# Performance work log

Measured on AMD Instinct MI355X. Metric: run time of the kernel, lower is better.

Reference implementation:

```python
import jax, jax.numpy as jnp
import numpy as np

LAMBDA_INIT = 0.8


def setup_inputs() -> dict:
    key = jax.random.key(0)
    ks = jax.random.split(key, 12)
    B, T, E = 2, 2048, 1024
    H = 8            # num_heads // 2 diff-heads
    HS = 64          # head_size
    DO = 128         # 2 * head_output_dimension (per-head output dim)
    q = jax.random.normal(ks[0], (B, T, E), jnp.float32)
    k = jax.random.normal(ks[1], (B, T, E), jnp.float32)
    v = jax.random.normal(ks[2], (B, T, E), jnp.float32)
    s = E ** -0.5  # linear-layer style init scale
    Wq = jax.random.normal(ks[3], (H, E, 2 * HS), jnp.float32) * s
    Wk = jax.random.normal(ks[4], (H, E, 2 * HS), jnp.float32) * s
    Wv = jax.random.normal(ks[5], (H, E, DO), jnp.float32) * s
    # lambda reparam vectors (scaled 0.1 to keep exp(dot) numerically tame)
    lq1 = jax.random.normal(ks[6], (H, HS), jnp.float32) * 0.1
    lk1 = jax.random.normal(ks[7], (H, HS), jnp.float32) * 0.1
    lq2 = jax.random.normal(ks[8], (H, HS), jnp.float32) * 0.1
    lk2 = jax.random.normal(ks[9], (H, HS), jnp.float32) * 0.1
    Wp = jax.random.normal(ks[10], (H * DO, E), jnp.float32) * (H * DO) ** -0.5
    bp = jnp.zeros((E,), jnp.float32)
    # buffer: tril(ones, diagonal=1); positions where it is 0 get -inf
    mask = jnp.tril(jnp.ones((T, T), jnp.bool_), 1)
    return {"q": q, "k": k, "v": v, "Wq": Wq, "Wk": Wk, "Wv": Wv,
            "lq1": lq1, "lk1": lk1, "lq2": lq2, "lk2": lk2,
            "Wp": Wp, "bp": bp, "mask": mask}


def reference(q, k, v, Wq, Wk, Wv, lq1, lk1, lq2, lk2, Wp, bp, mask):
    B, T, E = q.shape
    H = Wq.shape[0]
    HS = Wq.shape[-1] // 2
    scale = HS ** -0.5
    Q = jnp.einsum('bte,hed->bhtd', q, Wq)   # [B,H,T,2HS]
    K = jnp.einsum('bte,hed->bhtd', k, Wk)
    V = jnp.einsum('bte,hed->bhtd', v, Wv)   # [B,H,T,DO]
    Q1, Q2 = jnp.split(Q, 2, axis=-1)
    K1, K2 = jnp.split(K, 2, axis=-1)
    neg_inf = jnp.float32(-jnp.inf)
    s1 = jnp.einsum('bhtd,bhsd->bhts', Q1, K1) * scale
    s2 = jnp.einsum('bhtd,bhsd->bhts', Q2, K2) * scale
    s1 = jnp.where(mask[:T, :T], s1, neg_inf)
    s2 = jnp.where(mask[:T, :T], s2, neg_inf)
    a1 = jax.nn.softmax(s1, axis=-1)
    a2 = jax.nn.softmax(s2, axis=-1)
    lbd = (jnp.exp(jnp.sum(lq1 * lk1, -1)) - jnp.exp(jnp.sum(lq2 * lk2, -1))
           + LAMBDA_INIT)                     # [H]
    attn = a1 - lbd[None, :, None, None] * a2
    ctx = jnp.einsum('bhts,bhsd->bhtd', attn, V) * (1.0 - LAMBDA_INIT)
    out = ctx.transpose(0, 2, 1, 3).reshape(B, T, -1)  # concat heads
    return out @ Wp + bp
```

## Files before the change

kernel.cpp:

```cpp
#include <hip/hip_runtime.h>
#include <hip/hip_bf16.h>


constexpr int Tn = 2048;
constexpr int En = 1024;
constexpr int Hn = 8;
constexpr float LAMBDA_INIT = 0.8f;
constexpr float QSCALE = 0.18033688011112042f;

typedef __attribute__((ext_vector_type(8))) short short8;
typedef __attribute__((ext_vector_type(4))) short s16x4;
typedef __attribute__((ext_vector_type(4))) float f32x4;

__device__ __forceinline__ short f2bf(float x) {
  union { __hip_bfloat16 h; short s; } u;
  u.h = __float2bfloat16(x);
  return u.s;
}
__device__ __forceinline__ void gload16(const short* g, short* l) {
  __builtin_amdgcn_global_load_lds(
      (const __attribute__((address_space(1))) void*)g,
      (__attribute__((address_space(3))) void*)l, 16, 0, 0);
}

__global__ __launch_bounds__(256)
void qkv_mfma(const float* __restrict__ q, const float* __restrict__ k,
              const float* __restrict__ v,
              const float* __restrict__ Wq, const float* __restrict__ Wk,
              const float* __restrict__ Wv,
              short* __restrict__ Qo, short* __restrict__ Ko,
              short* __restrict__ Vto) {
  __shared__ short As[2][128 * 32];
  __shared__ short Bs[2][128 * 32];
  const int which = blockIdx.z;
  const float* X = (which == 0) ? q : (which == 1) ? k : v;
  const float* W = (which == 0) ? Wq : (which == 1) ? Wk : Wv;
  const int head = blockIdx.y;
  const int m0 = blockIdx.x * 128;
  const float* Wh = W + (size_t)head * En * 128;
  const float oscale = (which == 0) ? QSCALE : 1.0f;

  const int tid = threadIdx.x;
  const int lane = tid & 63;
  const int w = tid >> 6, wr = w >> 1, wc = w & 1;
  const int fr = lane & 15, fk = (lane >> 4) * 8;
  const int arow = tid >> 1, ah = (tid & 1) * 16;
  const int bn = tid & 127, bkg = (tid >> 7) * 16;

  float4 xa[4];
  float xb[16];

  auto gload = [&](int k0) {
#pragma unroll
    for (int qq = 0; qq < 4; ++qq)
      xa[qq] = *(const float4*)&X[(size_t)(m0 + arow) * En + k0 + ah + qq * 4];
#pragma unroll
    for (int j = 0; j < 16; ++j)
      xb[j] = Wh[(size_t)(k0 + bkg + j) * 128 + bn];
  };
  auto cvtwrite = [&](int buf) {
    short8 pa0, pa1;
#pragma unroll
    for (int e = 0; e < 4; ++e) {
      pa0[e]     = f2bf(((const float*)&xa[0])[e]);
      pa0[e + 4] = f2bf(((const float*)&xa[1])[e]);
      pa1[e]     = f2bf(((const float*)&xa[2])[e]);
      pa1[e + 4] = f2bf(((const float*)&xa[3])[e]);
    }
    *(short8*)&As[buf][arow * 32 + ah] = pa0;
    *(short8*)&As[buf][arow * 32 + ah + 8] = pa1;
    short8 pb0, pb1;
#pragma unroll
    for (int e = 0; e < 8; ++e) {
      pb0[e] = f2bf(xb[e]);
      pb1[e] = f2bf(xb[e + 8]);
    }
    *(short8*)&Bs[buf][bn * 32 + bkg] = pb0;
    *(short8*)&Bs[buf][bn * 32 + bkg + 8] = pb1;
  };

  f32x4 acc[4][4] = {};
  gload(0);
  cvtwrite(0);
  gload(32);
  __syncthreads();

  for (int k0 = 0; k0 < En; k0 += 32) {
    const int cur = (k0 >> 5) & 1;
    if (k0 + 32 < En) {
      cvtwrite(cur ^ 1);
      if (k0 + 64 < En) gload(k0 + 64);
    }
    short8 a[4], b[4];
#pragma unroll
    for (int i = 0; i < 4; ++i)
      a[i] = *(const short8*)&As[cur][(wr * 64 + i * 16 + fr) * 32 + fk];
#pragma unroll
    for (int j = 0; j < 4; ++j)
      b[j] = *(const short8*)&Bs[cur][(wc * 64 + j * 16 + fr) * 32 + fk];
#pragma unroll
    for (int i = 0; i < 4; ++i)
#pragma unroll
      for (int j = 0; j < 4; ++j)
        acc[i][j] = __builtin_amdgcn_mfma_f32_16x16x32_bf16(a[i], b[j],
                                                            acc[i][j], 0, 0, 0);
    __syncthreads();
  }

  const int crow = (lane >> 4) * 4, ccol = lane & 15;
  if (which == 2) {
#pragma unroll
    for (int i = 0; i < 4; ++i) {
      const int m = m0 + wr * 64 + i * 16 + crow;
      const int bb = m >> 11, t = m & (Tn - 1);
#pragma unroll
      for (int j = 0; j < 4; ++j) {
        const int d = wc * 64 + j * 16 + ccol;
        s16x4 pk;
#pragma unroll
        for (int p = 0; p < 4; ++p) pk[p] = f2bf(acc[i][j][p]);
        *(s16x4*)&Vto[((size_t)(bb * Hn + head) * 128 + d) * Tn + t] = pk;
      }
    }
  } else {
    short* Out = (which == 0) ? Qo : Ko;
#pragma unroll
    for (int i = 0; i < 4; ++i) {
      const int m = m0 + wr * 64 + i * 16 + crow;
      const int bb = m >> 11, t = m & (Tn - 1);
      short* dst = Out + ((size_t)(bb * Hn + head) * Tn + t) * 128;
#pragma unroll
      for (int j = 0; j < 4; ++j) {
        const int d = wc * 64 + j * 16 + ccol;
#pragma unroll
        for (int p = 0; p < 4; ++p)
          dst[(size_t)p * 128 + d] = f2bf(acc[i][j][p] * oscale);
      }
    }
  }
}

__global__ __launch_bounds__(256)
void proj_mfma(const short* __restrict__ Xb, const float* __restrict__ W,
               const float* __restrict__ bias, float* __restrict__ Out) {
  __shared__ short As[2][64 * 32];
  __shared__ short Bs[2][128 * 32];
  const int m0 = blockIdx.x * 64;
  const int n0 = blockIdx.y * 128;

  const int tid = threadIdx.x;
  const int lane = tid & 63;
  const int w = tid >> 6, wr = w >> 1, wc = w & 1;
  const int fr = lane & 15, fk = (lane >> 4) * 8;
  const int arow = tid >> 2, ah = (tid & 3) * 8;
  const int bn = tid & 127, bkg = (tid >> 7) * 16;

  short8 xa8;
  float xb[16];

  auto gload = [&](int k0) {
    xa8 = *(const short8*)&Xb[(size_t)(m0 + arow) * En + k0 + ah];
#pragma unroll
    for (int j = 0; j < 16; ++j)
      xb[j] = W[(size_t)(k0 + bkg + j) * En + n0 + bn];
  };
  auto cvtwrite = [&](int buf) {
    *(short8*)&As[buf][arow * 32 + ah] = xa8;
    short8 pb0, pb1;
#pragma unroll
    for (int e = 0; e < 8; ++e) {
      pb0[e] = f2bf(xb[e]);
      pb1[e] = f2bf(xb[e + 8]);
    }
    *(short8*)&Bs[buf][bn * 32 + bkg] = pb0;
    *(short8*)&Bs[buf][bn * 32 + bkg + 8] = pb1;
  };

  f32x4 acc[2][4] = {};
  gload(0);
  cvtwrite(0);
  gload(32);
  __syncthreads();

  for (int k0 = 0; k0 < En; k0 += 32) {
    const int cur = (k0 >> 5) & 1;
    if (k0 + 32 < En) {
      cvtwrite(cur ^ 1);
      if (k0 + 64 < En) gload(k0 + 64);
    }
    short8 a[2], b[4];
#pragma unroll
    for (int i = 0; i < 2; ++i)
      a[i] = *(const short8*)&As[cur][(wr * 32 + i * 16 + fr) * 32 + fk];
#pragma unroll
    for (int j = 0; j < 4; ++j)
      b[j] = *(const short8*)&Bs[cur][(wc * 64 + j * 16 + fr) * 32 + fk];
#pragma unroll
    for (int i = 0; i < 2; ++i)
#pragma unroll
      for (int j = 0; j < 4; ++j)
        acc[i][j] = __builtin_amdgcn_mfma_f32_16x16x32_bf16(a[i], b[j],
                                                            acc[i][j], 0, 0, 0);
    __syncthreads();
  }

  const int crow = (lane >> 4) * 4, ccol = lane & 15;
#pragma unroll
  for (int i = 0; i < 2; ++i) {
    const int m = m0 + wr * 32 + i * 16 + crow;
#pragma unroll
    for (int j = 0; j < 4; ++j) {
      const int n = n0 + wc * 64 + j * 16 + ccol;
      const float bv = bias[n];
#pragma unroll
      for (int p = 0; p < 4; ++p)
        Out[(size_t)(m + p) * En + n] = acc[i][j][p] + bv;
    }
  }
}

__global__ __launch_bounds__(256, 4)
void diff_attn7(const short* __restrict__ Qg, const short* __restrict__ Kg,
                const short* __restrict__ Vtg,
                const float* __restrict__ lq1, const float* __restrict__ lk1,
                const float* __restrict__ lq2, const float* __restrict__ lk2,
                short* __restrict__ ctxb) {
  __shared__ __align__(16) short pool[18688];

  const int lin = blockIdx.x;
  const int h = lin & 7;
  const int idx = lin >> 3;
  const int b = idx >> 5;
  const int x = idx & 31;
  const int tid = threadIdx.x;
  const int lane = tid & 63;
  const int w = tid >> 6;
  const int st = w >> 1, wh = w & 1;
  const int fr = lane & 15, hi = lane >> 4;
  const int swz = fr & 7;
  const int swv = (fr ^ (fr >> 2)) & 3;
  const size_t basebh = (size_t)(b * Hn + h) * Tn * 128;

  float lbd;
  {
    float a1 = lq1[h * 64 + lane] * lk1[h * 64 + lane];
    float a2 = lq2[h * 64 + lane] * lk2[h * 64 + lane];
#pragma unroll
    for (int off = 1; off <= 32; off <<= 1) {
      a1 += __shfl_xor(a1, off);
      a2 += __shfl_xor(a2, off);
    }
    lbd = __expf(a1) - __expf(a2) + LAMBDA_INIT;
  }

  int ksrc[2], vsrc[2], dsto[2];
#pragma unroll
  for (int j = 0; j < 2; ++j) {
    const int ob = j * 4096 + tid * 16;
    { const int s = ob >> 8, cp = (ob >> 4) & 15, c = cp ^ (s & 7);
      ksrc[j] = s * 128 + c * 8; }
    { const int d = ob >> 6, cp = (ob >> 4) & 3,
          c = cp ^ ((d ^ (d >> 2)) & 3);
      vsrc[j] = d * Tn + c * 8; }
    dsto[j] = (j * 4096 + w * 1024) >> 1;
  }
  const short* kgb = Kg + basebh;
  const short* vgb = Vtg + basebh;

#define STAGE(BUF, S0)                                                   \
  {                                                                      \
    const short* kb_ = kgb + (size_t)(S0) * 128;                         \
    const short* vb_ = vgb + (S0);                                       \
    _Pragma("unroll") for (int j = 0; j < 2; ++j) {                      \
      gload16(kb_ + ksrc[j], pool + (BUF) * 4096 + dsto[j]);             \
      gload16(vb_ + vsrc[j], pool + 8192 + (BUF) * 4096 + dsto[j]);      \
    }                                                                    \
  }

  short8 ones;
#pragma unroll
  for (int e = 0; e < 8; ++e) ones[e] = (short)0x3F80;
  short* Plw = pool + 16384 + w * 576;

  auto phase = [&](int qi) {
    const int q0 = qi * 32;
    const int NT = min(Tn / 32, qi + 2);
    const int tmin = q0 + wh * 16;
    const int tbase = tmin + hi * 4;

    short8 qf[2];
    {
      const short* qp = Qg + basebh + (size_t)(tmin + fr) * 128 + st * 64;
      qf[0] = *(const short8*)(qp + hi * 8);
      qf[1] = *(const short8*)(qp + 32 + hi * 8);
    }
    f32x4 o[8] = {};
    f32x4 ol = {};

    STAGE(0, 0);
    int cur = 0;
    for (int t = 0; t < NT; ++t) {
      const int s0 = t * 32;
      if (t + 1 < NT) {
        STAGE(cur ^ 1, s0 + 32);
        __builtin_amdgcn_sched_barrier(0);
        asm volatile("s_waitcnt vmcnt(4)" ::: "memory");
        __builtin_amdgcn_sched_barrier(0);
      } else {
        __builtin_amdgcn_sched_barrier(0);
        asm volatile("s_waitcnt vmcnt(0)" ::: "memory");
        __builtin_amdgcn_sched_barrier(0);
      }
      __builtin_amdgcn_s_barrier();

      if (s0 <= tmin + 16) {
        const short* Kb = pool + cur * 4096;
        const short* Vb = pool + 8192 + cur * 4096;
        const bool interior = (tmin - s0) >= 30;

        f32x4 s4[2] = {};
        __builtin_amdgcn_s_setprio(1);
#pragma unroll
        for (int sb = 0; sb < 2; ++sb) {
          const int rb = (sb * 16 + fr) * 128;
#pragma unroll
          for (int kp = 0; kp < 2; ++kp) {
            const short8 kb = *(const short8*)
                &Kb[rb + ((st * 8 + ((kp * 4 + hi) ^ swz)) << 3)];
            s4[sb] = __builtin_amdgcn_mfma_f32_16x16x32_bf16(qf[kp], kb,
                                                             s4[sb], 0, 0, 0);
          }
        }
        __builtin_amdgcn_s_setprio(0);
        if (!interior) {
#pragma unroll
          for (int sb = 0; sb < 2; ++sb) {
            const int sg = s0 + sb * 16 + fr;
#pragma unroll
            for (int p = 0; p < 4; ++p)
              if (sg > tbase + p + 1) s4[sb][p] = -1e30f;
          }
        }

#pragma unroll
        for (int sb = 0; sb < 2; ++sb)
#pragma unroll
          for (int p = 0; p < 4; ++p)
            Plw[(hi * 4 + p) * 36 + sb * 16 + fr] =
                f2bf(exp2f(s4[sb][p] - 12.0f));

        const short8 pf = *(const short8*)&Plw[fr * 36 + hi * 8];
        __builtin_amdgcn_s_setprio(1);
        ol = __builtin_amdgcn_mfma_f32_16x16x32_bf16(ones, pf, ol, 0, 0, 0);
#pragma unroll
        for (int dblk = 0; dblk < 8; ++dblk) {
          const short8 va = *(const short8*)
              &Vb[(dblk * 16 + fr) * 32 + ((hi ^ swv) << 3)];
          o[dblk] = __builtin_amdgcn_mfma_f32_16x16x32_bf16(va, pf, o[dblk],
                                                            0, 0, 0);
        }
        __builtin_amdgcn_s_setprio(0);
      }

      __builtin_amdgcn_s_barrier();
      cur ^= 1;
    }

    const float lr = ol[0];
    float* O2L = (float*)pool;
    if (st == 1) {
      const float c2 = (1.0f - LAMBDA_INIT) * lbd / lr;
#pragma unroll
      for (int dblk = 0; dblk < 8; ++dblk)
#pragma unroll
        for (int e = 0; e < 4; ++e)
          O2L[wh * 2176 + (dblk * 16 + hi * 4 + e) * 17 + fr] =
              c2 * o[dblk][e];
    }
    __syncthreads();
    if (st == 0) {
      const float c1 = (1.0f - LAMBDA_INIT) / lr;
      const int t = tmin + fr;
      short* dst = ctxb + ((size_t)b * Tn + t) * En + h * 128;
#pragma unroll
      for (int dblk = 0; dblk < 8; ++dblk) {
        s16x4 pk;
#pragma unroll
        for (int e = 0; e < 4; ++e)
          pk[e] = f2bf(c1 * o[dblk][e] -
                       O2L[wh * 2176 + (dblk * 16 + hi * 4 + e) * 17 + fr]);
        *(s16x4*)&dst[dblk * 16 + hi * 4] = pk;
      }
    }
    __syncthreads();
  };

  phase(63 - x);
  phase(x);
#undef STAGE
}

extern "C" void kernel_launch(void* const* d_in, const int* in_sizes, int n_in,
                              void* d_out, int out_size, void* d_ws, size_t ws_size,
                              hipStream_t stream) {
  const float* q   = (const float*)d_in[0];
  const float* k   = (const float*)d_in[1];
  const float* v   = (const float*)d_in[2];
  const float* Wq  = (const float*)d_in[3];
  const float* Wk  = (const float*)d_in[4];
  const float* Wv  = (const float*)d_in[5];
  const float* lq1 = (const float*)d_in[6];
  const float* lk1 = (const float*)d_in[7];
  const float* lq2 = (const float*)d_in[8];
  const float* lk2 = (const float*)d_in[9];
  const float* Wp  = (const float*)d_in[10];
  const float* bp  = (const float*)d_in[11];

  short* ws = (short*)d_ws;
  const size_t SZ = (size_t)2 * Hn * Tn * 128;
  short* Qb   = ws;
  short* Kb   = ws + SZ;
  short* Vtb  = ws + 2 * SZ;
  short* ctxb = ws + 3 * SZ;

  qkv_mfma<<<dim3(32, 8, 3), dim3(256), 0, stream>>>(q, k, v, Wq, Wk, Wv,
                                                     Qb, Kb, Vtb);
  diff_attn7<<<dim3(512), dim3(256), 0, stream>>>(Qb, Kb, Vtb,
                                                  lq1, lk1, lq2, lk2, ctxb);
  proj_mfma<<<dim3(64, 8), dim3(256), 0, stream>>>(ctxb, Wp, bp,
                                                   (float*)d_out);
}
```

Baseline: 161.3 us.

## Pre-convert inputs and weights to bf16, use direct global-to-LDS loads in GEMMs

Adds two prepass kernels: one converts q/k/v activations to bf16, and one transposes and converts all weight matrices to bf16 in K-contiguous layout. The QKV and projection GEMMs then stream tiles straight into LDS with global_load_lds, using explicit vmcnt waits and raw barriers, instead of loading fp32 into registers, converting and writing to LDS. This removes the uncoalesced strided weight loads and per-tile conversion work from the GEMM inner loops. In exchange it adds two extra launches and extra global traffic for the bf16 copies, and the weight conversion is redone on every call.

```diff
diff --git a/kernel.cpp b/kernel.cpp
--- a/kernel.cpp
+++ b/kernel.cpp
@@ -7,6 +7,8 @@
 constexpr int Hn = 8;
 constexpr float LAMBDA_INIT = 0.8f;
 constexpr float QSCALE = 0.18033688011112042f;
+constexpr size_t SZb = (size_t)2 * Tn * En;
+constexpr size_t WSZ = (size_t)En * En;
 
 typedef __attribute__((ext_vector_type(8))) short short8;
 typedef __attribute__((ext_vector_type(4))) short s16x4;
@@ -24,88 +26,132 @@
 }
 
 __global__ __launch_bounds__(256)
-void qkv_mfma(const float* __restrict__ q, const float* __restrict__ k,
-              const float* __restrict__ v,
-              const float* __restrict__ Wq, const float* __restrict__ Wk,
-              const float* __restrict__ Wv,
-              short* __restrict__ Qo, short* __restrict__ Ko,
-              short* __restrict__ Vto) {
-  __shared__ short As[2][128 * 32];
-  __shared__ short Bs[2][128 * 32];
+void cvt3(const float* __restrict__ q, const float* __restrict__ k,
+          const float* __restrict__ v, short* __restrict__ ws) {
+  const float* src = (blockIdx.y == 0) ? q : (blockIdx.y == 1) ? k : v;
+  short* dst = ws + (size_t)blockIdx.y * SZb;
+  const size_t i = ((size_t)blockIdx.x * 256 + threadIdx.x) * 8;
+  float4 a = *(const float4*)&src[i];
+  float4 b = *(const float4*)&src[i + 4];
+  short8 o;
+  o[0] = f2bf(a.x); o[1] = f2bf(a.y); o[2] = f2bf(a.z); o[3] = f2bf(a.w);
+  o[4] = f2bf(b.x); o[5] = f2bf(b.y); o[6] = f2bf(b.z); o[7] = f2bf(b.w);
+  *(short8*)&dst[i] = o;
+}
+
+__global__ __launch_bounds__(256)
+void twt(const float* __restrict__ Wq, const float* __restrict__ Wk,
+         const float* __restrict__ Wv, const float* __restrict__ Wp,
+         short* __restrict__ WT) {
+  __shared__ float tl[64][65];
+  const int id = blockIdx.x;
+  const int tid = threadIdx.x;
+  const float* src;
+  short* dst;
+  int r0, c0, C;
+  if (id < 768) {
+    const int wi = id >> 8;
+    const float* W = (wi == 0) ? Wq : (wi == 1) ? Wk : Wv;
+    const int rem = id & 255;
+    const int h = rem >> 5;
+    const int tile = rem & 31;
+    r0 = (tile >> 1) * 64;
+    c0 = (tile & 1) * 64;
+    C = 128;
+    src = W + (size_t)h * En * 128;
+    dst = WT + (size_t)wi * WSZ + (size_t)h * 128 * En;
+  } else {
+    const int idx = id - 768;
+    r0 = (idx >> 4) * 64;
+    c0 = (idx & 15) * 64;
+    C = En;
+    src = Wp;
+    dst = WT + 3 * WSZ;
+  }
+  const int r = tid >> 2, cc = (tid & 3) * 16;
+#pragma unroll
+  for (int j = 0; j < 4; ++j) {
+    const float4 x = *(const float4*)&src[(size_t)(r0 + r) * C + c0 + cc + j * 4];
+    tl[r][cc + j * 4 + 0] = x.x;
+    tl[r][cc + j * 4 + 1] = x.y;
+    tl[r][cc + j * 4 + 2] = x.z;
+    tl[r][cc + j * 4 + 3] = x.w;
+  }
+  __syncthreads();
+  const int c = tid >> 2, rc = (tid & 3) * 16;
+  short8 o0, o1;
+#pragma unroll
+  for (int e = 0; e < 8; ++e) {
+    o0[e] = f2bf(tl[rc + e][c]);
+    o1[e] = f2bf(tl[rc + 8 + e][c]);
+  }
+  *(short8*)&dst[(size_t)(c0 + c) * En + r0 + rc] = o0;
+  *(short8*)&dst[(size_t)(c0 + c) * En + r0 + rc + 8] = o1;
+}
+
+__global__ __launch_bounds__(256)
+void qkv_mfma2(const short* __restrict__ Xq, const short* __restrict__ Xk,
+               const short* __restrict__ Xv, const short* __restrict__ WT,
+               short* __restrict__ Qo, short* __restrict__ Ko,
+               short* __restrict__ Vto) {
+  __shared__ __align__(16) short As[2][4096];
+  __shared__ __align__(16) short Bs2[2][4096];
   const int which = blockIdx.z;
-  const float* X = (which == 0) ? q : (which == 1) ? k : v;
-  const float* W = (which == 0) ? Wq : (which == 1) ? Wk : Wv;
+  const short* X = (which == 0) ? Xq : (which == 1) ? Xk : Xv;
   const int head = blockIdx.y;
   const int m0 = blockIdx.x * 128;
-  const float* Wh = W + (size_t)head * En * 128;
+  const short* Bt = WT + (size_t)which * WSZ + (size_t)head * 128 * En;
   const float oscale = (which == 0) ? QSCALE : 1.0f;
 
   const int tid = threadIdx.x;
   const int lane = tid & 63;
   const int w = tid >> 6, wr = w >> 1, wc = w & 1;
   const int fr = lane & 15, fk = (lane >> 4) * 8;
-  const int arow = tid >> 1, ah = (tid & 1) * 16;
-  const int bn = tid & 127, bkg = (tid >> 7) * 16;
-
-  float4 xa[4];
-  float xb[16];
-
-  auto gload = [&](int k0) {
-#pragma unroll
-    for (int qq = 0; qq < 4; ++qq)
-      xa[qq] = *(const float4*)&X[(size_t)(m0 + arow) * En + k0 + ah + qq * 4];
-#pragma unroll
-    for (int j = 0; j < 16; ++j)
-      xb[j] = Wh[(size_t)(k0 + bkg + j) * 128 + bn];
-  };
-  auto cvtwrite = [&](int buf) {
-    short8 pa0, pa1;
-#pragma unroll
-    for (int e = 0; e < 4; ++e) {
-      pa0[e]     = f2bf(((const float*)&xa[0])[e]);
-      pa0[e + 4] = f2bf(((const float*)&xa[1])[e]);
-      pa1[e]     = f2bf(((const float*)&xa[2])[e]);
-      pa1[e + 4] = f2bf(((const float*)&xa[3])[e]);
-    }
-    *(short8*)&As[buf][arow * 32 + ah] = pa0;
-    *(short8*)&As[buf][arow * 32 + ah + 8] = pa1;
-    short8 pb0, pb1;
-#pragma unroll
-    for (int e = 0; e < 8; ++e) {
-      pb0[e] = f2bf(xb[e]);
-      pb1[e] = f2bf(xb[e + 8]);
-    }
-    *(short8*)&Bs[buf][bn * 32 + bkg] = pb0;
-    *(short8*)&Bs[buf][bn * 32 + bkg + 8] = pb1;
-  };
+  const int srow = tid >> 2, sch = (tid & 3) * 8;
+  const int wdst = w * 512;
+
+#define QSTAGE(BUF, K0)                                                  \
+  {                                                                      \
+    _Pragma("unroll") for (int j = 0; j < 2; ++j) {                      \
+      gload16(&X[(size_t)(m0 + j * 64 + srow) * En + (K0) + sch],        \
+              &As[BUF][j * 2048 + wdst]);                                \
+      gload16(&Bt[(size_t)(j * 64 + srow) * En + (K0) + sch],            \
+              &Bs2[BUF][j * 2048 + wdst]);                               \
+    }                                                                    \
+  }
 
   f32x4 acc[4][4] = {};
-  gload(0);
-  cvtwrite(0);
-  gload(32);
-  __syncthreads();
-
+  QSTAGE(0, 0);
   for (int k0 = 0; k0 < En; k0 += 32) {
     const int cur = (k0 >> 5) & 1;
     if (k0 + 32 < En) {
-      cvtwrite(cur ^ 1);
-      if (k0 + 64 < En) gload(k0 + 64);
-    }
+      QSTAGE(cur ^ 1, k0 + 32);
+      __builtin_amdgcn_sched_barrier(0);
+      asm volatile("s_waitcnt vmcnt(4)" ::: "memory");
+      __builtin_amdgcn_sched_barrier(0);
+    } else {
+      __builtin_amdgcn_sched_barrier(0);
+      asm volatile("s_waitcnt vmcnt(0)" ::: "memory");
+      __builtin_amdgcn_sched_barrier(0);
+    }
+    __builtin_amdgcn_s_barrier();
+
     short8 a[4], b[4];
 #pragma unroll
     for (int i = 0; i < 4; ++i)
       a[i] = *(const short8*)&As[cur][(wr * 64 + i * 16 + fr) * 32 + fk];
 #pragma unroll
     for (int j = 0; j < 4; ++j)
-      b[j] = *(const short8*)&Bs[cur][(wc * 64 + j * 16 + fr) * 32 + fk];
+      b[j] = *(const short8*)&Bs2[cur][(wc * 64 + j * 16 + fr) * 32 + fk];
 #pragma unroll
     for (int i = 0; i < 4; ++i)
 #pragma unroll
       for (int j = 0; j < 4; ++j)
         acc[i][j] = __builtin_amdgcn_mfma_f32_16x16x32_bf16(a[i], b[j],
                                                             acc[i][j], 0, 0, 0);
-    __syncthreads();
-  }
+    __builtin_amdgcn_s_barrier();
+  }
+#undef QSTAGE
 
   const int crow = (lane >> 4) * 4, ccol = lane & 15;
   if (which == 2) {
@@ -141,10 +187,10 @@
 }
 
 __global__ __launch_bounds__(256)
-void proj_mfma(const short* __restrict__ Xb, const float* __restrict__ W,
-               const float* __restrict__ bias, float* __restrict__ Out) {
-  __shared__ short As[2][64 * 32];
-  __shared__ short Bs[2][128 * 32];
+void proj_mfma2(const short* __restrict__ Xb, const short* __restrict__ WpT,
+                const float* __restrict__ bias, float* __restrict__ Out) {
+  __shared__ __align__(16) short As[2][2048];
+  __shared__ __align__(16) short Bs2[2][4096];
   const int m0 = blockIdx.x * 64;
   const int n0 = blockIdx.y * 128;
 
@@ -152,57 +198,50 @@
   const int lane = tid & 63;
   const int w = tid >> 6, wr = w >> 1, wc = w & 1;
   const int fr = lane & 15, fk = (lane >> 4) * 8;
-  const int arow = tid >> 2, ah = (tid & 3) * 8;
-  const int bn = tid & 127, bkg = (tid >> 7) * 16;
-
-  short8 xa8;
-  float xb[16];
-
-  auto gload = [&](int k0) {
-    xa8 = *(const short8*)&Xb[(size_t)(m0 + arow) * En + k0 + ah];
-#pragma unroll
-    for (int j = 0; j < 16; ++j)
-      xb[j] = W[(size_t)(k0 + bkg + j) * En + n0 + bn];
-  };
-  auto cvtwrite = [&](int buf) {
-    *(short8*)&As[buf][arow * 32 + ah] = xa8;
-    short8 pb0, pb1;
-#pragma unroll
-    for (int e = 0; e < 8; ++e) {
-      pb0[e] = f2bf(xb[e]);
-      pb1[e] = f2bf(xb[e + 8]);
-    }
-    *(short8*)&Bs[buf][bn * 32 + bkg] = pb0;
-    *(short8*)&Bs[buf][bn * 32 + bkg + 8] = pb1;
-  };
+  const int srow = tid >> 2, sch = (tid & 3) * 8;
+  const int wdst = w * 512;
+
+#define PSTAGE(BUF, K0)                                                  \
+  {                                                                      \
+    gload16(&Xb[(size_t)(m0 + srow) * En + (K0) + sch],                  \
+            &As[BUF][wdst]);                                             \
+    _Pragma("unroll") for (int j = 0; j < 2; ++j)                        \
+      gload16(&WpT[(size_t)(n0 + j * 64 + srow) * En + (K0) + sch],      \
+              &Bs2[BUF][j * 2048 + wdst]);                               \
+  }
 
   f32x4 acc[2][4] = {};
-  gload(0);
-  cvtwrite(0);
-  gload(32);
-  __syncthreads();
-
+  PSTAGE(0, 0);
   for (int k0 = 0; k0 < En; k0 += 32) {
     const int cur = (k0 >> 5) & 1;
     if (k0 + 32 < En) {
-      cvtwrite(cur ^ 1);
-      if (k0 + 64 < En) gload(k0 + 64);
-    }
+      PSTAGE(cur ^ 1, k0 + 32);
+      __builtin_amdgcn_sched_barrier(0);
+      asm volatile("s_waitcnt vmcnt(3)" ::: "memory");
+      __builtin_amdgcn_sched_barrier(0);
+    } else {
+      __builtin_amdgcn_sched_barrier(0);
+      asm volatile("s_waitcnt vmcnt(0)" ::: "memory");
+      __builtin_amdgcn_sched_barrier(0);
+    }
+    __builtin_amdgcn_s_barrier();
+
     short8 a[2], b[4];
 #pragma unroll
     for (int i = 0; i < 2; ++i)
       a[i] = *(const short8*)&As[cur][(wr * 32 + i * 16 + fr) * 32 + fk];
 #pragma unroll
     for (int j = 0; j < 4; ++j)
-      b[j] = *(const short8*)&Bs[cur][(wc * 64 + j * 16 + fr) * 32 + fk];
+      b[j] = *(const short8*)&Bs2[cur][(wc * 64 + j * 16 + fr) * 32 + fk];
 #pragma unroll
     for (int i = 0; i < 2; ++i)
 #pragma unroll
       for (int j = 0; j < 4; ++j)
         acc[i][j] = __builtin_amdgcn_mfma_f32_16x16x32_bf16(a[i], b[j],
                                                             acc[i][j], 0, 0, 0);
-    __syncthreads();
-  }
+    __builtin_amdgcn_s_barrier();
+  }
+#undef PSTAGE
 
   const int crow = (lane >> 4) * 4, ccol = lane & 15;
 #pragma unroll
@@ -417,16 +456,21 @@
   const float* bp  = (const float*)d_in[11];
 
   short* ws = (short*)d_ws;
-  const size_t SZ = (size_t)2 * Hn * Tn * 128;
-  short* Qb   = ws;
-  short* Kb   = ws + SZ;
-  short* Vtb  = ws + 2 * SZ;
-  short* ctxb = ws + 3 * SZ;
-
-  qkv_mfma<<<dim3(32, 8, 3), dim3(256), 0, stream>>>(q, k, v, Wq, Wk, Wv,
-                                                     Qb, Kb, Vtb);
+  short* qbf = ws;
+  short* kbf = ws + SZb;
+  short* vbf = ws + 2 * SZb;
+  short* Qb  = ws + 3 * SZb;
+  short* Kb  = ws + 4 * SZb;
+  short* Vtb = ws + 5 * SZb;
+  short* WT  = ws + 6 * SZb;
+  short* ctxb = qbf;
+
+  cvt3<<<dim3(2048, 3), dim3(256), 0, stream>>>(q, k, v, ws);
+  twt<<<dim3(1024), dim3(256), 0, stream>>>(Wq, Wk, Wv, Wp, WT);
+  qkv_mfma2<<<dim3(32, 8, 3), dim3(256), 0, stream>>>(qbf, kbf, vbf, WT,
+                                                      Qb, Kb, Vtb);
   diff_attn7<<<dim3(512), dim3(256), 0, stream>>>(Qb, Kb, Vtb,
                                                   lq1, lk1, lq2, lk2, ctxb);
-  proj_mfma<<<dim3(64, 8), dim3(256), 0, stream>>>(ctxb, Wp, bp,
-                                                   (float*)d_out);
-}
+  proj_mfma2<<<dim3(64, 8), dim3(256), 0, stream>>>(ctxb, WT + 3 * WSZ, bp,
+                                                    (float*)d_out);
+}
```

Result: faster. 143.7 us (-10.9%).
